# Kernel optimization log

Measured on AMD Instinct MI355X. Metric: run time of the kernel, lower is better.

The kernel has to match this reference:

```python
import jax, jax.numpy as jnp
import numpy as np

V, E, H, TAGS, T = 100000, 300, 512, 25, 2048
NEG = -10000.0


def _lstm_dir(x, w_ih, w_hh, b_ih, b_hh, reverse):
    # x: [T, din]; PyTorch gate order i, f, g, o. Single sequence (batch=1 squeezed).
    def step(carry, xt):
        h, c = carry
        gates = xt @ w_ih.T + b_ih + h @ w_hh.T + b_hh  # [4H]
        i_, f_, g_, o_ = jnp.split(gates, 4)
        i_ = jax.nn.sigmoid(i_)
        f_ = jax.nn.sigmoid(f_)
        g_ = jnp.tanh(g_)
        o_ = jax.nn.sigmoid(o_)
        c = f_ * c + i_ * g_
        h = o_ * jnp.tanh(c)
        return (h, c), h
    h0 = jnp.zeros((H,), x.dtype)
    _, hs = jax.lax.scan(step, (h0, h0), x, reverse=reverse)
    return hs  # [T, H]


def _bilstm_layer(x, wf_ih, wf_hh, bf_ih, bf_hh, wb_ih, wb_hh, bb_ih, bb_hh):
    hf = _lstm_dir(x, wf_ih, wf_hh, bf_ih, bf_hh, reverse=False)
    hb = _lstm_dir(x, wb_ih, wb_hh, bb_ih, bb_hh, reverse=True)
    return jnp.concatenate([hf, hb], axis=-1)  # [T, 2H]


def _viterbi(feats, transitions):
    # feats: [T, TAGS]; transitions[next, prev]
    fv0 = jnp.full((TAGS,), NEG, feats.dtype).at[0].set(0.0)

    def vstep(fv, feat):
        scores = fv[None, :] + transitions        # [next, prev]
        bp = jnp.argmax(scores, axis=1)            # [TAGS]
        fv = jnp.max(scores, axis=1) + feat        # [TAGS]
        return fv, bp

    fv, bps = jax.lax.scan(vstep, fv0, feats)      # bps: [T, TAGS]
    best = jnp.argmax(fv)

    def back(tag, bp):
        return bp[tag], tag

    _, path = jax.lax.scan(back, best, bps, reverse=True)
    return path  # [T] int tags, times 0..T-1


def setup_inputs() -> dict:
    key = jax.random.key(0)
    ks = jax.random.split(key, 24)

    def g(k, shape, scale=0.05):
        return jax.random.normal(k, shape, dtype=jnp.float32) * scale

    inp = {}
    inp["sentence"] = jax.random.randint(ks[0], (1, T), 0, V)
    inp["embedding"] = g(ks[1], (V, E))
    i = 2
    for layer, din in ((0, E), (1, 2 * H)):
        for d in ("f", "b"):
            inp[f"w_ih_l{layer}_{d}"] = g(ks[i], (4 * H, din)); i += 1
            inp[f"w_hh_l{layer}_{d}"] = g(ks[i], (4 * H, H)); i += 1
            inp[f"b_ih_l{layer}_{d}"] = g(ks[i], (4 * H,)); i += 1
            inp[f"b_hh_l{layer}_{d}"] = g(ks[i], (4 * H,)); i += 1
    inp["w_tag"] = g(ks[18], (TAGS, 2 * H))
    inp["b_tag"] = g(ks[19], (TAGS,))
    inp["transitions"] = jax.random.normal(ks[20], (TAGS, TAGS), dtype=jnp.float32)
    return inp


def reference(sentence, embedding,
              w_ih_l0_f, w_hh_l0_f, b_ih_l0_f, b_hh_l0_f,
              w_ih_l0_b, w_hh_l0_b, b_ih_l0_b, b_hh_l0_b,
              w_ih_l1_f, w_hh_l1_f, b_ih_l1_f, b_hh_l1_f,
              w_ih_l1_b, w_hh_l1_b, b_ih_l1_b, b_hh_l1_b,
              w_tag, b_tag, transitions):
    x = embedding[sentence[0]]  # [T, E] (batch=1, squeezed as in original)
    h1 = _bilstm_layer(x, w_ih_l0_f, w_hh_l0_f, b_ih_l0_f, b_hh_l0_f,
                       w_ih_l0_b, w_hh_l0_b, b_ih_l0_b, b_hh_l0_b)
    h2 = _bilstm_layer(h1, w_ih_l1_f, w_hh_l1_f, b_ih_l1_f, b_hh_l1_f,
                       w_ih_l1_b, w_hh_l1_b, b_ih_l1_b, b_hh_l1_b)
    feats = h2 @ w_tag.T + b_tag  # [T, TAGS]
    return _viterbi(feats, transitions)
```

## Files before the change

kernel.cpp:

```cpp
#include <hip/hip_runtime.h>
#include <cmath>

#define TT   2048
#define EE   300
#define HH   512
#define G4H  2048
#define NTAG 25
#define NEGV (-10000.0f)
#define LWG  32
#define POISON 0xFFBADBADu

__device__ __forceinline__ float fsig(float x)  { return 1.f / (1.f + __expf(-x)); }
__device__ __forceinline__ float ftanh(float x) { return 1.f - 2.f / (__expf(2.f * x) + 1.f); }

__global__ void poison_kernel(uint32_t* __restrict__ p, int n) {
    int i = blockIdx.x * blockDim.x + threadIdx.x;
    for (; i < n; i += gridDim.x * blockDim.x) p[i] = POISON;
}

__global__ void embed_kernel(const int* __restrict__ sent,
                             const float* __restrict__ emb,
                             float* __restrict__ x) {
    int t = blockIdx.x;
    int row = sent[t];
    const float4* src = (const float4*)(emb + (size_t)row * EE);
    float4* dst = (float4*)(x + (size_t)t * EE);
    for (int i = threadIdx.x; i < EE / 4; i += blockDim.x) dst[i] = src[i];
}

#define BM 64
#define BN 64
#define BKK 16
__global__ __launch_bounds__(256)
void gemm_abt(const float* __restrict__ A, int lda,
              const float* __restrict__ B, int ldb,
              const float* __restrict__ bias1,
              const float* __restrict__ bias2,
              float* __restrict__ C, int ldc,
              int M, int N, int K) {
    __shared__ float As[BKK][BM + 4];
    __shared__ float Bs[BKK][BN + 4];
    const int tid = threadIdx.x;
    const int tx = tid & 15, ty = tid >> 4;
    const int bm = blockIdx.x * BM, bn = blockIdx.y * BN;
    float acc[4][4] = {};
    for (int k0 = 0; k0 < K; k0 += BKK) {
        #pragma unroll
        for (int i = 0; i < 4; ++i) {
            int m = (tid >> 4) + i * 16;
            int k = tid & 15;
            float a = 0.f, b = 0.f;
            if (k0 + k < K) {
                if (bm + m < M) a = A[(size_t)(bm + m) * lda + k0 + k];
                if (bn + m < N) b = B[(size_t)(bn + m) * ldb + k0 + k];
            }
            As[k][m] = a;
            Bs[k][m] = b;
        }
        __syncthreads();
        #pragma unroll
        for (int k = 0; k < BKK; ++k) {
            float4 a4 = *(const float4*)&As[k][ty * 4];
            float4 b4 = *(const float4*)&Bs[k][tx * 4];
            acc[0][0] += a4.x * b4.x; acc[0][1] += a4.x * b4.y;
            acc[0][2] += a4.x * b4.z; acc[0][3] += a4.x * b4.w;
            acc[1][0] += a4.y * b4.x; acc[1][1] += a4.y * b4.y;
            acc[1][2] += a4.y * b4.z; acc[1][3] += a4.y * b4.w;
            acc[2][0] += a4.z * b4.x; acc[2][1] += a4.z * b4.y;
            acc[2][2] += a4.z * b4.z; acc[2][3] += a4.z * b4.w;
            acc[3][0] += a4.w * b4.x; acc[3][1] += a4.w * b4.y;
            acc[3][2] += a4.w * b4.z; acc[3][3] += a4.w * b4.w;
        }
        __syncthreads();
    }
    #pragma unroll
    for (int i = 0; i < 4; ++i) {
        int m = bm + ty * 4 + i;
        if (m < M) {
            #pragma unroll
            for (int j = 0; j < 4; ++j) {
                int n = bn + tx * 4 + j;
                if (n < N) {
                    float v = acc[i][j];
                    if (bias1) v += bias1[n];
                    if (bias2) v += bias2[n];
                    C[(size_t)m * ldc + n] = v;
                }
            }
        }
    }
}

#define GM 128
#define GN 128
#define GK 16
__global__ __launch_bounds__(256)
void gemm128(const float* __restrict__ A, int lda,
             const float* __restrict__ B, int ldb,
             const float* __restrict__ bias1,
             const float* __restrict__ bias2,
             float* __restrict__ C, int ldc, int K) {
    __shared__ float As[GK][GM + 4];
    __shared__ float Bs[GK][GN + 4];
    const int tid = threadIdx.x;
    const int tx = tid & 15, ty = tid >> 4;
    const int bm = blockIdx.x * GM, bn = blockIdx.y * GN;
    const int lm = tid >> 1, lkq = (tid & 1) * 8;
    float acc[8][8] = {};
    for (int k0 = 0; k0 < K; k0 += GK) {
        float4 a0 = *(const float4*)&A[(size_t)(bm + lm) * lda + k0 + lkq];
        float4 a1 = *(const float4*)&A[(size_t)(bm + lm) * lda + k0 + lkq + 4];
        float4 b0 = *(const float4*)&B[(size_t)(bn + lm) * ldb + k0 + lkq];
        float4 b1 = *(const float4*)&B[(size_t)(bn + lm) * ldb + k0 + lkq + 4];
        As[lkq + 0][lm] = a0.x; As[lkq + 1][lm] = a0.y;
        As[lkq + 2][lm] = a0.z; As[lkq + 3][lm] = a0.w;
        As[lkq + 4][lm] = a1.x; As[lkq + 5][lm] = a1.y;
        As[lkq + 6][lm] = a1.z; As[lkq + 7][lm] = a1.w;
        Bs[lkq + 0][lm] = b0.x; Bs[lkq + 1][lm] = b0.y;
        Bs[lkq + 2][lm] = b0.z; Bs[lkq + 3][lm] = b0.w;
        Bs[lkq + 4][lm] = b1.x; Bs[lkq + 5][lm] = b1.y;
        Bs[lkq + 6][lm] = b1.z; Bs[lkq + 7][lm] = b1.w;
        __syncthreads();
        #pragma unroll
        for (int k = 0; k < GK; ++k) {
            float4 x0 = *(const float4*)&As[k][ty * 8];
            float4 x1 = *(const float4*)&As[k][ty * 8 + 4];
            float4 y0 = *(const float4*)&Bs[k][tx * 8];
            float4 y1 = *(const float4*)&Bs[k][tx * 8 + 4];
            float xa[8] = {x0.x, x0.y, x0.z, x0.w, x1.x, x1.y, x1.z, x1.w};
            float yb[8] = {y0.x, y0.y, y0.z, y0.w, y1.x, y1.y, y1.z, y1.w};
            #pragma unroll
            for (int i = 0; i < 8; ++i)
                #pragma unroll
                for (int j = 0; j < 8; ++j)
                    acc[i][j] += xa[i] * yb[j];
        }
        __syncthreads();
    }
    #pragma unroll
    for (int i = 0; i < 8; ++i) {
        int m = bm + ty * 8 + i;
        float* cr = C + (size_t)m * ldc + bn + tx * 8;
        #pragma unroll
        for (int j = 0; j < 8; ++j) {
            float v = acc[i][j];
            int n = bn + tx * 8 + j;
            if (bias1) v += bias1[n];
            if (bias2) v += bias2[n];
            cr[j] = v;
        }
    }
}

__global__ __launch_bounds__(512, 1)
void lstm_kernel(const float* __restrict__ gx,
                 const float* __restrict__ whh_f,
                 const float* __restrict__ whh_b,
                 float* __restrict__ gates,
                 float* __restrict__ hout)
{
    const int tid = threadIdx.x;
    const int dir = blockIdx.x >> 5;
    const int wg  = blockIdx.x & 31;
    const int r   = tid >> 3;
    const int cch = tid & 7;
    const int gb  = r >> 4;
    const int ur  = r & 15;
    const int grow = gb * HH + wg * 16 + ur;
    const float* W = dir ? whh_b : whh_f;

    float4 w[16];
    {
        const float4* wr = (const float4*)(W + (size_t)grow * HH);
        #pragma unroll
        for (int i = 0; i < 16; ++i) w[i] = wr[cch + 8 * i];
    }
    #pragma unroll
    for (int i = 0; i < 16; ++i)
        asm volatile("" : "+v"(w[i].x), "+v"(w[i].y), "+v"(w[i].z), "+v"(w[i].w));

    __shared__ float h_s[HH];

    float c = 0.f;
    uint32_t* gbuf = (uint32_t*)(gates + (size_t)dir * TT * G4H);
    const float* gxd = gx + (size_t)dir * TT * G4H;

    float gxc = 0.f, gxn = 0.f, gxf = 0.f;
    if (cch == 0) {
        int t0 = dir ? TT - 1 : 0;
        int t1 = dir ? TT - 2 : 1;
        gxc = gxd[(size_t)t0 * G4H + grow];
        gxn = gxd[(size_t)t1 * G4H + grow];
    }

    for (int s = 0; s <= TT; ++s) {
        if (s > 0) {
            const uint32_t* gp = gbuf + (size_t)(s - 1) * G4H + tid;
            uint32_t v0, v1, v2, v3;
            for (;;) {
                v0 = __hip_atomic_load(gp,        __ATOMIC_RELAXED, __HIP_MEMORY_SCOPE_AGENT);
                v1 = __hip_atomic_load(gp + 512,  __ATOMIC_RELAXED, __HIP_MEMORY_SCOPE_AGENT);
                v2 = __hip_atomic_load(gp + 1024, __ATOMIC_RELAXED, __HIP_MEMORY_SCOPE_AGENT);
                v3 = __hip_atomic_load(gp + 1536, __ATOMIC_RELAXED, __HIP_MEMORY_SCOPE_AGENT);
                if ((v0 != POISON) & (v1 != POISON) & (v2 != POISON) & (v3 != POISON)) break;
            }
            float gi = fsig(__uint_as_float(v0));
            float gf = fsig(__uint_as_float(v1));
            float gg = ftanh(__uint_as_float(v2));
            float go = fsig(__uint_as_float(v3));
            c = gf * c + gi * gg;
            float h = go * ftanh(c);
            h_s[tid] = h;
            if (wg == 0) {
                int tp = dir ? (TT - s) : (s - 1);
                hout[(size_t)tp * (2 * HH) + dir * HH + tid] = h;
            }
        } else {
            h_s[tid] = 0.f;
        }
        if (s == TT) break;

        if (cch == 0) {
            gxf = 0.f;
            if (s + 2 < TT) {
                int tf = dir ? (TT - 1 - (s + 2)) : (s + 2);
                gxf = gxd[(size_t)tf * G4H + grow];
            }
        }
        __syncthreads();

        float a0 = 0.f, a1 = 0.f, a2 = 0.f, a3 = 0.f;
        const float4* h4 = (const float4*)h_s;
        #pragma unroll
        for (int i = 0; i < 16; i += 4) {
            float4 p0 = h4[cch + 8 * (i + 0)];
            float4 p1 = h4[cch + 8 * (i + 1)];
            float4 p2 = h4[cch + 8 * (i + 2)];
            float4 p3 = h4[cch + 8 * (i + 3)];
            a0 += w[i + 0].x * p0.x + w[i + 0].y * p0.y + w[i + 0].z * p0.z + w[i + 0].w * p0.w;
            a1 += w[i + 1].x * p1.x + w[i + 1].y * p1.y + w[i + 1].z * p1.z + w[i + 1].w * p1.w;
            a2 += w[i + 2].x * p2.x + w[i + 2].y * p2.y + w[i + 2].z * p2.z + w[i + 2].w * p2.w;
            a3 += w[i + 3].x * p3.x + w[i + 3].y * p3.y + w[i + 3].z * p3.z + w[i + 3].w * p3.w;
        }
        float acc = (a0 + a1) + (a2 + a3);
        acc += __shfl_xor(acc, 1);
        acc += __shfl_xor(acc, 2);
        acc += __shfl_xor(acc, 4);
        if (cch == 0)
            __hip_atomic_store(gbuf + (size_t)s * G4H + grow,
                               __float_as_uint(acc + gxc),
                               __ATOMIC_RELAXED, __HIP_MEMORY_SCOPE_AGENT);
        __syncthreads();
        gxc = gxn; gxn = gxf;
    }
}

__global__ void viterbi_kernel(const float* __restrict__ feats,
                               const float* __restrict__ trans,
                               int* __restrict__ bp,
                               int* __restrict__ out) {
    const int n = threadIdx.x;
    __shared__ float fv_s[NTAG];
    float tr[NTAG];
    if (n < NTAG) {
        #pragma unroll
        for (int p = 0; p < NTAG; ++p) tr[p] = trans[n * NTAG + p];
    }
    float fv = (n == 0) ? 0.f : NEGV;
    for (int t = 0; t < TT; ++t) {
        if (n < NTAG) fv_s[n] = fv;
        __syncthreads();
        if (n < NTAG) {
            float best = -INFINITY; int bb = 0;
            #pragma unroll
            for (int p = 0; p < NTAG; ++p) {
                float sc = fv_s[p] + tr[p];
                if (sc > best) { best = sc; bb = p; }
            }
            bp[t * NTAG + n] = bb;
            fv = best + feats[t * NTAG + n];
        }
        __syncthreads();
    }
    if (n < NTAG) fv_s[n] = fv;
    __syncthreads();
    if (n == 0) {
        float best = -INFINITY; int tag = 0;
        for (int p = 0; p < NTAG; ++p)
            if (fv_s[p] > best) { best = fv_s[p]; tag = p; }
        for (int t = TT - 1; t >= 0; --t) {
            out[t] = tag;
            tag = bp[t * NTAG + tag];
        }
    }
}

extern "C" void kernel_launch(void* const* d_in, const int* in_sizes, int n_in,
                              void* d_out, int out_size, void* d_ws, size_t ws_size,
                              hipStream_t stream) {
    const int*   sent      = (const int*)d_in[0];
    const float* emb       = (const float*)d_in[1];
    const float* w_ih_l0_f = (const float*)d_in[2];
    const float* w_hh_l0_f = (const float*)d_in[3];
    const float* b_ih_l0_f = (const float*)d_in[4];
    const float* b_hh_l0_f = (const float*)d_in[5];
    const float* w_ih_l0_b = (const float*)d_in[6];
    const float* w_hh_l0_b = (const float*)d_in[7];
    const float* b_ih_l0_b = (const float*)d_in[8];
    const float* b_hh_l0_b = (const float*)d_in[9];
    const float* w_ih_l1_f = (const float*)d_in[10];
    const float* w_hh_l1_f = (const float*)d_in[11];
    const float* b_ih_l1_f = (const float*)d_in[12];
    const float* b_hh_l1_f = (const float*)d_in[13];
    const float* w_ih_l1_b = (const float*)d_in[14];
    const float* w_hh_l1_b = (const float*)d_in[15];
    const float* b_ih_l1_b = (const float*)d_in[16];
    const float* b_hh_l1_b = (const float*)d_in[17];
    const float* w_tag     = (const float*)d_in[18];
    const float* b_tag     = (const float*)d_in[19];
    const float* trans     = (const float*)d_in[20];

    char* ws = (char*)d_ws;
    float* x     = (float*)(ws);
    float* gx    = (float*)(ws + 2457600);
    float* gates = (float*)(ws + 36012032);
    float* h1    = (float*)(ws + 69566464);
    float* h2    = (float*)(ws + 77955072);
    float* feats = (float*)(ws + 86343680);
    int*   bp    = (int*)  (ws + 86548480);

    const int NGATES = 2 * TT * G4H;

    poison_kernel<<<2048, 256, 0, stream>>>((uint32_t*)gates, NGATES);

    embed_kernel<<<TT, 128, 0, stream>>>(sent, emb, x);

    dim3 g0(TT / BM, G4H / BN);
    gemm_abt<<<g0, 256, 0, stream>>>(x, EE, w_ih_l0_f, EE, b_ih_l0_f, b_hh_l0_f,
                                     gx, G4H, TT, G4H, EE);
    gemm_abt<<<g0, 256, 0, stream>>>(x, EE, w_ih_l0_b, EE, b_ih_l0_b, b_hh_l0_b,
                                     gx + (size_t)TT * G4H, G4H, TT, G4H, EE);
    lstm_kernel<<<64, 512, 0, stream>>>(gx, w_hh_l0_f, w_hh_l0_b, gates, h1);

    dim3 g1(TT / GM, G4H / GN);
    gemm128<<<g1, 256, 0, stream>>>(h1, 2 * HH, w_ih_l1_f, 2 * HH, b_ih_l1_f, b_hh_l1_f,
                                    gx, G4H, 2 * HH);
    gemm128<<<g1, 256, 0, stream>>>(h1, 2 * HH, w_ih_l1_b, 2 * HH, b_ih_l1_b, b_hh_l1_b,
                                    gx + (size_t)TT * G4H, G4H, 2 * HH);
    poison_kernel<<<2048, 256, 0, stream>>>((uint32_t*)gates, NGATES);
    lstm_kernel<<<64, 512, 0, stream>>>(gx, w_hh_l1_f, w_hh_l1_b, gates, h2);

    dim3 gf(TT / BM, 1);
    gemm_abt<<<gf, 256, 0, stream>>>(h2, 2 * HH, w_tag, 2 * HH, b_tag, nullptr,
                                     feats, NTAG, TT, NTAG, 2 * HH);

    viterbi_kernel<<<1, 64, 0, stream>>>(feats, trans, bp, (int*)d_out);
}
```

Baseline: 7.913 ms.

## Interleave forward and backward LSTM directions in one workgroup, keep Viterbi backpointers in LDS

The LSTM recurrence now uses 32 workgroups, each handling both directions. The forward step's cross-workgroup wait and matvec are interleaved with the backward step's, so one direction's global-memory sync latency can overlap the other's compute. Each wavefront now owns 4 gate rows with a full 32-lane reduction instead of 8-lane groups per row, which doubles weight registers per thread. Viterbi backpointers move from global ints to a byte array in shared memory to cut global traffic in the serial backtrace. The trade-offs are higher register pressure and fewer CUs doing the per-step matvec work.

```diff
diff --git a/kernel.cpp b/kernel.cpp
--- a/kernel.cpp
+++ b/kernel.cpp
@@ -7,11 +7,12 @@
 #define G4H  2048
 #define NTAG 25
 #define NEGV (-10000.0f)
-#define LWG  32
 #define POISON 0xFFBADBADu
 
 __device__ __forceinline__ float fsig(float x)  { return 1.f / (1.f + __expf(-x)); }
 __device__ __forceinline__ float ftanh(float x) { return 1.f - 2.f / (__expf(2.f * x) + 1.f); }
+__device__ __forceinline__ uint32_t f2u(float x) { return __float_as_uint(x); }
+__device__ __forceinline__ float u2f(uint32_t x) { return __uint_as_float(x); }
 
 __global__ void poison_kernel(uint32_t* __restrict__ p, int n) {
     int i = blockIdx.x * blockDim.x + threadIdx.x;
@@ -152,7 +153,7 @@
     }
 }
 
-__global__ __launch_bounds__(512, 1)
+__global__ __launch_bounds__(512, 2)
 void lstm_kernel(const float* __restrict__ gx,
                  const float* __restrict__ whh_f,
                  const float* __restrict__ whh_b,
@@ -160,107 +161,162 @@
                  float* __restrict__ hout)
 {
     const int tid = threadIdx.x;
-    const int dir = blockIdx.x >> 5;
-    const int wg  = blockIdx.x & 31;
-    const int r   = tid >> 3;
-    const int cch = tid & 7;
-    const int gb  = r >> 4;
-    const int ur  = r & 15;
-    const int grow = gb * HH + wg * 16 + ur;
-    const float* W = dir ? whh_b : whh_f;
-
-    float4 w[16];
-    {
-        const float4* wr = (const float4*)(W + (size_t)grow * HH);
-        #pragma unroll
-        for (int i = 0; i < 16; ++i) w[i] = wr[cch + 8 * i];
-    }
+    const int wg  = blockIdx.x;
+    const int g   = tid >> 5;
+    const int l   = tid & 31;
+    const int gb  = g >> 2;
+    const int growb = gb * HH + wg * 16 + (g & 3) * 4;
+
+    float4 wf[16], wb[16];
     #pragma unroll
-    for (int i = 0; i < 16; ++i)
-        asm volatile("" : "+v"(w[i].x), "+v"(w[i].y), "+v"(w[i].z), "+v"(w[i].w));
-
-    __shared__ float h_s[HH];
-
-    float c = 0.f;
-    uint32_t* gbuf = (uint32_t*)(gates + (size_t)dir * TT * G4H);
-    const float* gxd = gx + (size_t)dir * TT * G4H;
-
-    float gxc = 0.f, gxn = 0.f, gxf = 0.f;
-    if (cch == 0) {
-        int t0 = dir ? TT - 1 : 0;
-        int t1 = dir ? TT - 2 : 1;
-        gxc = gxd[(size_t)t0 * G4H + grow];
-        gxn = gxd[(size_t)t1 * G4H + grow];
+    for (int j = 0; j < 4; ++j) {
+        const float4* rf = (const float4*)(whh_f + (size_t)(growb + j) * HH);
+        const float4* rb = (const float4*)(whh_b + (size_t)(growb + j) * HH);
+        #pragma unroll
+        for (int i = 0; i < 4; ++i) {
+            wf[j * 4 + i] = rf[l + 32 * i];
+            wb[j * 4 + i] = rb[l + 32 * i];
+        }
+    }
+    #pragma unroll
+    for (int i = 0; i < 16; ++i) {
+        asm volatile("" : "+v"(wf[i].x), "+v"(wf[i].y), "+v"(wf[i].z), "+v"(wf[i].w));
+        asm volatile("" : "+v"(wb[i].x), "+v"(wb[i].y), "+v"(wb[i].z), "+v"(wb[i].w));
+    }
+
+    __shared__ float hf_s[HH];
+    __shared__ float hb_s[HH];
+
+    float cf = 0.f, cb = 0.f;
+    uint32_t* gfp = (uint32_t*)gates;
+    uint32_t* gbp = (uint32_t*)(gates + (size_t)TT * G4H);
+    const float* gxf = gx;
+    const float* gxb = gx + (size_t)TT * G4H;
+
+    float4 xfc{}, xfn{}, xff{}, xbc{}, xbn{}, xbf{};
+    if (l == 0) {
+        xfc = *(const float4*)(gxf + (size_t)0 * G4H + growb);
+        xfn = *(const float4*)(gxf + (size_t)1 * G4H + growb);
+        xbc = *(const float4*)(gxb + (size_t)(TT - 1) * G4H + growb);
+        xbn = *(const float4*)(gxb + (size_t)(TT - 2) * G4H + growb);
     }
 
     for (int s = 0; s <= TT; ++s) {
+        float hfv;
         if (s > 0) {
-            const uint32_t* gp = gbuf + (size_t)(s - 1) * G4H + tid;
+            const uint32_t* p = gfp + (size_t)(s - 1) * G4H + tid;
             uint32_t v0, v1, v2, v3;
             for (;;) {
-                v0 = __hip_atomic_load(gp,        __ATOMIC_RELAXED, __HIP_MEMORY_SCOPE_AGENT);
-                v1 = __hip_atomic_load(gp + 512,  __ATOMIC_RELAXED, __HIP_MEMORY_SCOPE_AGENT);
-                v2 = __hip_atomic_load(gp + 1024, __ATOMIC_RELAXED, __HIP_MEMORY_SCOPE_AGENT);
-                v3 = __hip_atomic_load(gp + 1536, __ATOMIC_RELAXED, __HIP_MEMORY_SCOPE_AGENT);
+                v0 = __hip_atomic_load(p,        __ATOMIC_RELAXED, __HIP_MEMORY_SCOPE_AGENT);
+                v1 = __hip_atomic_load(p + 512,  __ATOMIC_RELAXED, __HIP_MEMORY_SCOPE_AGENT);
+                v2 = __hip_atomic_load(p + 1024, __ATOMIC_RELAXED, __HIP_MEMORY_SCOPE_AGENT);
+                v3 = __hip_atomic_load(p + 1536, __ATOMIC_RELAXED, __HIP_MEMORY_SCOPE_AGENT);
                 if ((v0 != POISON) & (v1 != POISON) & (v2 != POISON) & (v3 != POISON)) break;
             }
-            float gi = fsig(__uint_as_float(v0));
-            float gf = fsig(__uint_as_float(v1));
-            float gg = ftanh(__uint_as_float(v2));
-            float go = fsig(__uint_as_float(v3));
-            c = gf * c + gi * gg;
-            float h = go * ftanh(c);
-            h_s[tid] = h;
-            if (wg == 0) {
-                int tp = dir ? (TT - s) : (s - 1);
-                hout[(size_t)tp * (2 * HH) + dir * HH + tid] = h;
-            }
+            float gi = fsig(u2f(v0));
+            float gf = fsig(u2f(v1));
+            float gg = ftanh(u2f(v2));
+            float go = fsig(u2f(v3));
+            cf = gf * cf + gi * gg;
+            hfv = go * ftanh(cf);
+            if (wg == 0) hout[(size_t)(s - 1) * (2 * HH) + tid] = hfv;
         } else {
-            h_s[tid] = 0.f;
-        }
-        if (s == TT) break;
-
-        if (cch == 0) {
-            gxf = 0.f;
-            if (s + 2 < TT) {
-                int tf = dir ? (TT - 1 - (s + 2)) : (s + 2);
-                gxf = gxd[(size_t)tf * G4H + grow];
-            }
-        }
-        __syncthreads();
-
-        float a0 = 0.f, a1 = 0.f, a2 = 0.f, a3 = 0.f;
-        const float4* h4 = (const float4*)h_s;
-        #pragma unroll
-        for (int i = 0; i < 16; i += 4) {
-            float4 p0 = h4[cch + 8 * (i + 0)];
-            float4 p1 = h4[cch + 8 * (i + 1)];
-            float4 p2 = h4[cch + 8 * (i + 2)];
-            float4 p3 = h4[cch + 8 * (i + 3)];
-            a0 += w[i + 0].x * p0.x + w[i + 0].y * p0.y + w[i + 0].z * p0.z + w[i + 0].w * p0.w;
-            a1 += w[i + 1].x * p1.x + w[i + 1].y * p1.y + w[i + 1].z * p1.z + w[i + 1].w * p1.w;
-            a2 += w[i + 2].x * p2.x + w[i + 2].y * p2.y + w[i + 2].z * p2.z + w[i + 2].w * p2.w;
-            a3 += w[i + 3].x * p3.x + w[i + 3].y * p3.y + w[i + 3].z * p3.z + w[i + 3].w * p3.w;
-        }
-        float acc = (a0 + a1) + (a2 + a3);
-        acc += __shfl_xor(acc, 1);
-        acc += __shfl_xor(acc, 2);
-        acc += __shfl_xor(acc, 4);
-        if (cch == 0)
-            __hip_atomic_store(gbuf + (size_t)s * G4H + grow,
-                               __float_as_uint(acc + gxc),
-                               __ATOMIC_RELAXED, __HIP_MEMORY_SCOPE_AGENT);
-        __syncthreads();
-        gxc = gxn; gxn = gxf;
+            hfv = 0.f;
+        }
+        hf_s[tid] = hfv;
+        __syncthreads();
+
+        if (s < TT) {
+            float a0 = 0.f, a1 = 0.f, a2 = 0.f, a3 = 0.f;
+            const float4* h4 = (const float4*)hf_s;
+            #pragma unroll
+            for (int i = 0; i < 4; ++i) {
+                float4 hv = h4[l + 32 * i];
+                a0 += wf[0 + i].x * hv.x + wf[0 + i].y * hv.y + wf[0 + i].z * hv.z + wf[0 + i].w * hv.w;
+                a1 += wf[4 + i].x * hv.x + wf[4 + i].y * hv.y + wf[4 + i].z * hv.z + wf[4 + i].w * hv.w;
+                a2 += wf[8 + i].x * hv.x + wf[8 + i].y * hv.y + wf[8 + i].z * hv.z + wf[8 + i].w * hv.w;
+                a3 += wf[12 + i].x * hv.x + wf[12 + i].y * hv.y + wf[12 + i].z * hv.z + wf[12 + i].w * hv.w;
+            }
+            #pragma unroll
+            for (int m = 1; m <= 16; m <<= 1) {
+                a0 += __shfl_xor(a0, m); a1 += __shfl_xor(a1, m);
+                a2 += __shfl_xor(a2, m); a3 += __shfl_xor(a3, m);
+            }
+            if (l == 0) {
+                uint32_t* q = gfp + (size_t)s * G4H + growb;
+                __hip_atomic_store(q + 0, f2u(a0 + xfc.x), __ATOMIC_RELAXED, __HIP_MEMORY_SCOPE_AGENT);
+                __hip_atomic_store(q + 1, f2u(a1 + xfc.y), __ATOMIC_RELAXED, __HIP_MEMORY_SCOPE_AGENT);
+                __hip_atomic_store(q + 2, f2u(a2 + xfc.z), __ATOMIC_RELAXED, __HIP_MEMORY_SCOPE_AGENT);
+                __hip_atomic_store(q + 3, f2u(a3 + xfc.w), __ATOMIC_RELAXED, __HIP_MEMORY_SCOPE_AGENT);
+                xff = make_float4(0.f, 0.f, 0.f, 0.f);
+                if (s + 2 < TT)
+                    xff = *(const float4*)(gxf + (size_t)(s + 2) * G4H + growb);
+            }
+        }
+
+        float hbv;
+        if (s > 0) {
+            const uint32_t* p = gbp + (size_t)(s - 1) * G4H + tid;
+            uint32_t v0, v1, v2, v3;
+            for (;;) {
+                v0 = __hip_atomic_load(p,        __ATOMIC_RELAXED, __HIP_MEMORY_SCOPE_AGENT);
+                v1 = __hip_atomic_load(p + 512,  __ATOMIC_RELAXED, __HIP_MEMORY_SCOPE_AGENT);
+                v2 = __hip_atomic_load(p + 1024, __ATOMIC_RELAXED, __HIP_MEMORY_SCOPE_AGENT);
+                v3 = __hip_atomic_load(p + 1536, __ATOMIC_RELAXED, __HIP_MEMORY_SCOPE_AGENT);
+                if ((v0 != POISON) & (v1 != POISON) & (v2 != POISON) & (v3 != POISON)) break;
+            }
+            float gi = fsig(u2f(v0));
+            float gf = fsig(u2f(v1));
+            float gg = ftanh(u2f(v2));
+            float go = fsig(u2f(v3));
+            cb = gf * cb + gi * gg;
+            hbv = go * ftanh(cb);
+            if (wg == 0) hout[(size_t)(TT - s) * (2 * HH) + HH + tid] = hbv;
+        } else {
+            hbv = 0.f;
+        }
+        hb_s[tid] = hbv;
+        __syncthreads();
+
+        if (s < TT) {
+            float a0 = 0.f, a1 = 0.f, a2 = 0.f, a3 = 0.f;
+            const float4* h4 = (const float4*)hb_s;
+            #pragma unroll
+            for (int i = 0; i < 4; ++i) {
+                float4 hv = h4[l + 32 * i];
+                a0 += wb[0 + i].x * hv.x + wb[0 + i].y * hv.y + wb[0 + i].z * hv.z + wb[0 + i].w * hv.w;
+                a1 += wb[4 + i].x * hv.x + wb[4 + i].y * hv.y + wb[4 + i].z * hv.z + wb[4 + i].w * hv.w;
+                a2 += wb[8 + i].x * hv.x + wb[8 + i].y * hv.y + wb[8 + i].z * hv.z + wb[8 + i].w * hv.w;
+                a3 += wb[12 + i].x * hv.x + wb[12 + i].y * hv.y + wb[12 + i].z * hv.z + wb[12 + i].w * hv.w;
+            }
+            #pragma unroll
+            for (int m = 1; m <= 16; m <<= 1) {
+                a0 += __shfl_xor(a0, m); a1 += __shfl_xor(a1, m);
+                a2 += __shfl_xor(a2, m); a3 += __shfl_xor(a3, m);
+            }
+            if (l == 0) {
+                uint32_t* q = gbp + (size_t)s * G4H + growb;
+                __hip_atomic_store(q + 0, f2u(a0 + xbc.x), __ATOMIC_RELAXED, __HIP_MEMORY_SCOPE_AGENT);
+                __hip_atomic_store(q + 1, f2u(a1 + xbc.y), __ATOMIC_RELAXED, __HIP_MEMORY_SCOPE_AGENT);
+                __hip_atomic_store(q + 2, f2u(a2 + xbc.z), __ATOMIC_RELAXED, __HIP_MEMORY_SCOPE_AGENT);
+                __hip_atomic_store(q + 3, f2u(a3 + xbc.w), __ATOMIC_RELAXED, __HIP_MEMORY_SCOPE_AGENT);
+                xbf = make_float4(0.f, 0.f, 0.f, 0.f);
+                if (s + 2 < TT)
+                    xbf = *(const float4*)(gxb + (size_t)(TT - 3 - s) * G4H + growb);
+            }
+        }
+
+        xfc = xfn; xfn = xff;
+        xbc = xbn; xbn = xbf;
     }
 }
 
 __global__ void viterbi_kernel(const float* __restrict__ feats,
                                const float* __restrict__ trans,
-                               int* __restrict__ bp,
                                int* __restrict__ out) {
     const int n = threadIdx.x;
     __shared__ float fv_s[NTAG];
+    __shared__ uint8_t bp_s[TT][NTAG];
     float tr[NTAG];
     if (n < NTAG) {
         #pragma unroll
@@ -277,7 +333,7 @@
                 float sc = fv_s[p] + tr[p];
                 if (sc > best) { best = sc; bb = p; }
             }
-            bp[t * NTAG + n] = bb;
+            bp_s[t][n] = (uint8_t)bb;
             fv = best + feats[t * NTAG + n];
         }
         __syncthreads();
@@ -290,7 +346,7 @@
             if (fv_s[p] > best) { best = fv_s[p]; tag = p; }
         for (int t = TT - 1; t >= 0; --t) {
             out[t] = tag;
-            tag = bp[t * NTAG + tag];
+            tag = bp_s[t][tag];
         }
     }
 }
@@ -327,7 +383,6 @@
     float* h1    = (float*)(ws + 69566464);
     float* h2    = (float*)(ws + 77955072);
     float* feats = (float*)(ws + 86343680);
-    int*   bp    = (int*)  (ws + 86548480);
 
     const int NGATES = 2 * TT * G4H;
 
@@ -340,7 +395,7 @@
                                      gx, G4H, TT, G4H, EE);
     gemm_abt<<<g0, 256, 0, stream>>>(x, EE, w_ih_l0_b, EE, b_ih_l0_b, b_hh_l0_b,
                                      gx + (size_t)TT * G4H, G4H, TT, G4H, EE);
-    lstm_kernel<<<64, 512, 0, stream>>>(gx, w_hh_l0_f, w_hh_l0_b, gates, h1);
+    lstm_kernel<<<32, 512, 0, stream>>>(gx, w_hh_l0_f, w_hh_l0_b, gates, h1);
 
     dim3 g1(TT / GM, G4H / GN);
     gemm128<<<g1, 256, 0, stream>>>(h1, 2 * HH, w_ih_l1_f, 2 * HH, b_ih_l1_f, b_hh_l1_f,
@@ -348,11 +403,11 @@
     gemm128<<<g1, 256, 0, stream>>>(h1, 2 * HH, w_ih_l1_b, 2 * HH, b_ih_l1_b, b_hh_l1_b,
                                     gx + (size_t)TT * G4H, G4H, 2 * HH);
     poison_kernel<<<2048, 256, 0, stream>>>((uint32_t*)gates, NGATES);
-    lstm_kernel<<<64, 512, 0, stream>>>(gx, w_hh_l1_f, w_hh_l1_b, gates, h2);
+    lstm_kernel<<<32, 512, 0, stream>>>(gx, w_hh_l1_f, w_hh_l1_b, gates, h2);
 
     dim3 gf(TT / BM, 1);
     gemm_abt<<<gf, 256, 0, stream>>>(h2, 2 * HH, w_tag, 2 * HH, b_tag, nullptr,
                                      feats, NTAG, TT, NTAG, 2 * HH);
 
-    viterbi_kernel<<<1, 64, 0, stream>>>(feats, trans, bp, (int*)d_out);
-}
+    viterbi_kernel<<<1, 64, 0, stream>>>(feats, trans, (int*)d_out);
+}
```

New measurement: 15.10 ms. +90.8%, slower.

## Interleave LSTM gate exchange buffer and poll with single 16-byte loads; keep Viterbi backpointers in LDS

Applied to the files above, without the earlier changes.

The gate exchange buffer is laid out as [t][unit][4 gates], so each consumer thread polls one 16-byte vector load that bypasses the cache instead of four separate atomic loads. The matvec mapping becomes 32 lanes per group of 4 rows with a wider shuffle reduction, so one writer lane stores four interleaved gates and loads a float4 of precomputed input terms. The Viterbi backpointers move from global int storage to a uint8 array in shared memory (about 51 KB), which removes global traffic from the serial backtrace. The inline asm cache bits and the moved barrier add ordering risk across workgroups.

```diff
diff --git a/kernel.cpp b/kernel.cpp
--- a/kernel.cpp
+++ b/kernel.cpp
@@ -7,11 +7,22 @@
 #define G4H  2048
 #define NTAG 25
 #define NEGV (-10000.0f)
-#define LWG  32
 #define POISON 0xFFBADBADu
+
+typedef uint32_t u32x4 __attribute__((ext_vector_type(4)));
 
 __device__ __forceinline__ float fsig(float x)  { return 1.f / (1.f + __expf(-x)); }
 __device__ __forceinline__ float ftanh(float x) { return 1.f - 2.f / (__expf(2.f * x) + 1.f); }
+__device__ __forceinline__ uint32_t f2u(float x) { return __float_as_uint(x); }
+__device__ __forceinline__ float u2f(uint32_t x) { return __uint_as_float(x); }
+
+__device__ __forceinline__ u32x4 poll16(const uint32_t* p) {
+    u32x4 v;
+    asm volatile("global_load_dwordx4 %0, %1, off sc0 sc1\n\t"
+                 "s_waitcnt vmcnt(0)"
+                 : "=v"(v) : "v"(p) : "memory");
+    return v;
+}
 
 __global__ void poison_kernel(uint32_t* __restrict__ p, int n) {
     int i = blockIdx.x * blockDim.x + threadIdx.x;
@@ -162,18 +173,19 @@
     const int tid = threadIdx.x;
     const int dir = blockIdx.x >> 5;
     const int wg  = blockIdx.x & 31;
-    const int r   = tid >> 3;
-    const int cch = tid & 7;
-    const int gb  = r >> 4;
-    const int ur  = r & 15;
-    const int grow = gb * HH + wg * 16 + ur;
+    const int g   = tid >> 5;
+    const int l   = tid & 31;
+    const int gb  = g >> 2;
+    const int u0  = wg * 16 + (g & 3) * 4;
+    const int growb = gb * HH + u0;
     const float* W = dir ? whh_b : whh_f;
 
     float4 w[16];
-    {
-        const float4* wr = (const float4*)(W + (size_t)grow * HH);
-        #pragma unroll
-        for (int i = 0; i < 16; ++i) w[i] = wr[cch + 8 * i];
+    #pragma unroll
+    for (int j = 0; j < 4; ++j) {
+        const float4* wr = (const float4*)(W + (size_t)(growb + j) * HH);
+        #pragma unroll
+        for (int i = 0; i < 4; ++i) w[j * 4 + i] = wr[l + 32 * i];
     }
     #pragma unroll
     for (int i = 0; i < 16; ++i)
@@ -182,32 +194,30 @@
     __shared__ float h_s[HH];
 
     float c = 0.f;
-    uint32_t* gbuf = (uint32_t*)(gates + (size_t)dir * TT * G4H);
+    uint32_t* gpd = (uint32_t*)gates + (size_t)dir * TT * G4H;
     const float* gxd = gx + (size_t)dir * TT * G4H;
 
-    float gxc = 0.f, gxn = 0.f, gxf = 0.f;
-    if (cch == 0) {
+    float4 xc{}, xn{}, xf{};
+    if (l == 0) {
         int t0 = dir ? TT - 1 : 0;
         int t1 = dir ? TT - 2 : 1;
-        gxc = gxd[(size_t)t0 * G4H + grow];
-        gxn = gxd[(size_t)t1 * G4H + grow];
+        xc = *(const float4*)(gxd + (size_t)t0 * G4H + growb);
+        xn = *(const float4*)(gxd + (size_t)t1 * G4H + growb);
     }
 
     for (int s = 0; s <= TT; ++s) {
         if (s > 0) {
-            const uint32_t* gp = gbuf + (size_t)(s - 1) * G4H + tid;
-            uint32_t v0, v1, v2, v3;
+            const uint32_t* p = gpd + ((size_t)(s - 1) * HH + tid) * 4;
+            u32x4 v;
             for (;;) {
-                v0 = __hip_atomic_load(gp,        __ATOMIC_RELAXED, __HIP_MEMORY_SCOPE_AGENT);
-                v1 = __hip_atomic_load(gp + 512,  __ATOMIC_RELAXED, __HIP_MEMORY_SCOPE_AGENT);
-                v2 = __hip_atomic_load(gp + 1024, __ATOMIC_RELAXED, __HIP_MEMORY_SCOPE_AGENT);
-                v3 = __hip_atomic_load(gp + 1536, __ATOMIC_RELAXED, __HIP_MEMORY_SCOPE_AGENT);
-                if ((v0 != POISON) & (v1 != POISON) & (v2 != POISON) & (v3 != POISON)) break;
-            }
-            float gi = fsig(__uint_as_float(v0));
-            float gf = fsig(__uint_as_float(v1));
-            float gg = ftanh(__uint_as_float(v2));
-            float go = fsig(__uint_as_float(v3));
+                v = poll16(p);
+                if ((v.x != POISON) & (v.y != POISON) &
+                    (v.z != POISON) & (v.w != POISON)) break;
+            }
+            float gi = fsig(u2f(v.x));
+            float gf = fsig(u2f(v.y));
+            float gg = ftanh(u2f(v.z));
+            float go = fsig(u2f(v.w));
             c = gf * c + gi * gg;
             float h = go * ftanh(c);
             h_s[tid] = h;
@@ -218,49 +228,50 @@
         } else {
             h_s[tid] = 0.f;
         }
+        __syncthreads();
         if (s == TT) break;
 
-        if (cch == 0) {
-            gxf = 0.f;
+        if (l == 0) {
+            xf = make_float4(0.f, 0.f, 0.f, 0.f);
             if (s + 2 < TT) {
-                int tf = dir ? (TT - 1 - (s + 2)) : (s + 2);
-                gxf = gxd[(size_t)tf * G4H + grow];
-            }
-        }
-        __syncthreads();
+                int tf = dir ? (TT - 3 - s) : (s + 2);
+                xf = *(const float4*)(gxd + (size_t)tf * G4H + growb);
+            }
+        }
 
         float a0 = 0.f, a1 = 0.f, a2 = 0.f, a3 = 0.f;
         const float4* h4 = (const float4*)h_s;
         #pragma unroll
-        for (int i = 0; i < 16; i += 4) {
-            float4 p0 = h4[cch + 8 * (i + 0)];
-            float4 p1 = h4[cch + 8 * (i + 1)];
-            float4 p2 = h4[cch + 8 * (i + 2)];
-            float4 p3 = h4[cch + 8 * (i + 3)];
-            a0 += w[i + 0].x * p0.x + w[i + 0].y * p0.y + w[i + 0].z * p0.z + w[i + 0].w * p0.w;
-            a1 += w[i + 1].x * p1.x + w[i + 1].y * p1.y + w[i + 1].z * p1.z + w[i + 1].w * p1.w;
-            a2 += w[i + 2].x * p2.x + w[i + 2].y * p2.y + w[i + 2].z * p2.z + w[i + 2].w * p2.w;
-            a3 += w[i + 3].x * p3.x + w[i + 3].y * p3.y + w[i + 3].z * p3.z + w[i + 3].w * p3.w;
-        }
-        float acc = (a0 + a1) + (a2 + a3);
-        acc += __shfl_xor(acc, 1);
-        acc += __shfl_xor(acc, 2);
-        acc += __shfl_xor(acc, 4);
-        if (cch == 0)
-            __hip_atomic_store(gbuf + (size_t)s * G4H + grow,
-                               __float_as_uint(acc + gxc),
-                               __ATOMIC_RELAXED, __HIP_MEMORY_SCOPE_AGENT);
-        __syncthreads();
-        gxc = gxn; gxn = gxf;
+        for (int i = 0; i < 4; ++i) {
+            float4 hv = h4[l + 32 * i];
+            a0 += w[0  + i].x * hv.x + w[0  + i].y * hv.y + w[0  + i].z * hv.z + w[0  + i].w * hv.w;
+            a1 += w[4  + i].x * hv.x + w[4  + i].y * hv.y + w[4  + i].z * hv.z + w[4  + i].w * hv.w;
+            a2 += w[8  + i].x * hv.x + w[8  + i].y * hv.y + w[8  + i].z * hv.z + w[8  + i].w * hv.w;
+            a3 += w[12 + i].x * hv.x + w[12 + i].y * hv.y + w[12 + i].z * hv.z + w[12 + i].w * hv.w;
+        }
+        #pragma unroll
+        for (int m = 1; m <= 16; m <<= 1) {
+            a0 += __shfl_xor(a0, m); a1 += __shfl_xor(a1, m);
+            a2 += __shfl_xor(a2, m); a3 += __shfl_xor(a3, m);
+        }
+        if (l == 0) {
+            uint32_t* q = gpd + ((size_t)s * HH + u0) * 4 + gb;
+            __hip_atomic_store(q + 0,  f2u(a0 + xc.x), __ATOMIC_RELAXED, __HIP_MEMORY_SCOPE_AGENT);
+            __hip_atomic_store(q + 4,  f2u(a1 + xc.y), __ATOMIC_RELAXED, __HIP_MEMORY_SCOPE_AGENT);
+            __hip_atomic_store(q + 8,  f2u(a2 + xc.z), __ATOMIC_RELAXED, __HIP_MEMORY_SCOPE_AGENT);
+            __hip_atomic_store(q + 12, f2u(a3 + xc.w), __ATOMIC_RELAXED, __HIP_MEMORY_SCOPE_AGENT);
+        }
+        __syncthreads();
+        xc = xn; xn = xf;
     }
 }
 
 __global__ void viterbi_kernel(const float* __restrict__ feats,
                                const float* __restrict__ trans,
-                               int* __restrict__ bp,
                                int* __restrict__ out) {
     const int n = threadIdx.x;
     __shared__ float fv_s[NTAG];
+    __shared__ uint8_t bp_s[TT][NTAG];
     float tr[NTAG];
     if (n < NTAG) {
         #pragma unroll
@@ -277,7 +288,7 @@
                 float sc = fv_s[p] + tr[p];
                 if (sc > best) { best = sc; bb = p; }
             }
-            bp[t * NTAG + n] = bb;
+            bp_s[t][n] = (uint8_t)bb;
             fv = best + feats[t * NTAG + n];
         }
         __syncthreads();
@@ -290,7 +301,7 @@
             if (fv_s[p] > best) { best = fv_s[p]; tag = p; }
         for (int t = TT - 1; t >= 0; --t) {
             out[t] = tag;
-            tag = bp[t * NTAG + tag];
+            tag = bp_s[t][tag];
         }
     }
 }
@@ -327,7 +338,6 @@
     float* h1    = (float*)(ws + 69566464);
     float* h2    = (float*)(ws + 77955072);
     float* feats = (float*)(ws + 86343680);
-    int*   bp    = (int*)  (ws + 86548480);
 
     const int NGATES = 2 * TT * G4H;
 
@@ -354,5 +364,5 @@
     gemm_abt<<<gf, 256, 0, stream>>>(h2, 2 * HH, w_tag, 2 * HH, b_tag, nullptr,
                                      feats, NTAG, TT, NTAG, 2 * HH);
 
-    viterbi_kernel<<<1, 64, 0, stream>>>(feats, trans, bp, (int*)d_out);
-}
+    viterbi_kernel<<<1, 64, 0, stream>>>(feats, trans, (int*)d_out);
+}
```

After: 11.14 ms. +40.7%, slower.
